# Kernel tuning notes

Hardware: AMD Instinct MI355X
Metric: run time of the kernel (lower is better)

## Reference

```python
import jax, jax.numpy as jnp
import numpy as np


def setup_inputs() -> dict:
    key = jax.random.key(0)
    kx, ky = jax.random.split(key)
    N, M, D = 16384, 16384, 512
    x = jax.random.normal(kx, (N, D), dtype=jnp.float32)
    y = jax.random.normal(ky, (M, D), dtype=jnp.float32)
    return {"x": x, "y": y, "device": 0}


def reference(x, y, device):
    # torch.cdist(x, y, p=2): pairwise Euclidean distances [N, M]
    # matching torch's large-matrix cdist path), clamped for numerical safety.
    x_sq = jnp.sum(x * x, axis=1, keepdims=True)          # [N, 1]
    y_sq = jnp.sum(y * y, axis=1)                          # [M]
    sq_dists = x_sq + y_sq[None, :] - 2.0 * (x @ y.T)      # [N, M]
    dists = jnp.sqrt(jnp.maximum(sq_dists, 0.0))
    # min over centers (dim=1), then argmax over candidates (dim=0)
    min_dists = jnp.min(dists, axis=1)                     # [N]
    max_id = jnp.argmax(min_dists)
    max_val = min_dists[max_id]
    return max_val, max_id
```

## Files before the change

### kernel.cpp

```cpp
#include <hip/hip_runtime.h>
#include <hip/hip_fp8.h>
#include <math.h>

#define N_ROWS 16384
#define M_ROWS 16384
#define DIM    512
#define JS     8
#define KCAND  256
#define DELTA  0.40f

typedef __attribute__((ext_vector_type(8))) int   int8v;
typedef __attribute__((ext_vector_type(4))) int   int4v;
typedef __attribute__((ext_vector_type(4))) float floatx4;

__global__ __launch_bounds__(256) void convert_kernel(const float* __restrict__ x, const float* __restrict__ y,
                                                      unsigned char* __restrict__ xh8, unsigned char* __restrict__ yh8,
                                                      float* __restrict__ x_sq, float* __restrict__ y_sq,
                                                      unsigned int* __restrict__ gmax_bits,
                                                      unsigned int* __restrict__ cnt, int* __restrict__ cand) {
    if (blockIdx.x == 0) {
        if (threadIdx.x < KCAND) cand[threadIdx.x] = 0;
        if (threadIdx.x == 0) { *gmax_bits = 0u; *cnt = 0u; }
    }
    int wave = threadIdx.x >> 6, lane = threadIdx.x & 63;
    int row = blockIdx.x * 4 + wave;
    const float* src; unsigned char* dst8; float* dsq; int r;
    if (row < N_ROWS) { r = row;          src = x; dst8 = xh8; dsq = x_sq; }
    else              { r = row - N_ROWS; src = y; dst8 = yh8; dsq = y_sq; }
    const float4* s4 = (const float4*)(src + (size_t)r * DIM);
    float4 a = s4[lane * 2];
    float4 b = s4[lane * 2 + 1];
    float v[8] = {a.x, a.y, a.z, a.w, b.x, b.y, b.z, b.w};
    union { unsigned char b[8]; uint2 u2; } pk;
    float s = 0.f;
    #pragma unroll
    for (int i = 0; i < 8; ++i) {
        s += v[i] * v[i];
        __hip_fp8_e4m3 q(v[i]);
        pk.b[i] = (unsigned char)q.__x;
    }
    *(uint2*)(dst8 + (size_t)r * DIM + lane * 8) = pk.u2;
    #pragma unroll
    for (int off = 32; off > 0; off >>= 1) s += __shfl_down(s, off, 64);
    if (lane == 0) dsq[r] = s;
}

__device__ __forceinline__ int8v read_frag(const unsigned char* base, int row, int quad) {
    int s = row & 7;
    int c0 = ((quad << 1) | 0) ^ s;
    int c1 = ((quad << 1) | 1) ^ s;
    int4v lo = *(const int4v*)(base + row * 128 + c0 * 16);
    int4v hi = *(const int4v*)(base + row * 128 + c1 * 16);
    int8v r;
    r[0] = lo[0]; r[1] = lo[1]; r[2] = lo[2]; r[3] = lo[3];
    r[4] = hi[0]; r[5] = hi[1]; r[6] = hi[2]; r[7] = hi[3];
    return r;
}

__global__ __launch_bounds__(256) void pass1_kernel(const unsigned char* __restrict__ xh8,
                                                    const unsigned char* __restrict__ yh8,
                                                    const float* __restrict__ y_sq,
                                                    float* __restrict__ part) {
    __shared__ __align__(16) unsigned char As[128 * 128];
    __shared__ __align__(16) unsigned char Bs[128 * 128];
    __shared__ float red[2][128];

    const int t = threadIdx.x;
    const int wid = t >> 6, lane = t & 63;
    const int wm = wid >> 1, wn = wid & 1;
    const int col = lane & 15, quad = lane >> 4;
    const int i0 = blockIdx.x * 128;
    const int jsplit = blockIdx.y;

    const unsigned char* sSrc = (wid < 2) ? xh8 : yh8;
    unsigned char* sDst = (wid < 2) ? As : Bs;
    const int sBase = (wid & 1) * 64;
    const int rr = lane >> 3;
    const int p  = lane & 7;
    const int srcChunkOff = ((p ^ rr) << 4);

    float minv[16];
    #pragma unroll
    for (int i = 0; i < 16; ++i) minv[i] = __builtin_inff();

    for (int jt = 0; jt < (M_ROWS / JS) / 128; ++jt) {
        const int j0 = jsplit * (M_ROWS / JS) + jt * 128;
        const int gBase = (wid < 2) ? i0 : j0;
        floatx4 acc[4][4];
        #pragma unroll
        for (int mt = 0; mt < 4; ++mt)
            #pragma unroll
            for (int nt = 0; nt < 4; ++nt) acc[mt][nt] = (floatx4){0.f, 0.f, 0.f, 0.f};

        for (int kc = 0; kc < DIM; kc += 128) {
            #pragma unroll
            for (int r = 0; r < 8; ++r) {
                const unsigned char* gp = sSrc + (size_t)(gBase + sBase + r * 8 + rr) * DIM + kc + srcChunkOff;
                unsigned char* lp = sDst + (sBase + r * 8) * 128;
                __builtin_amdgcn_global_load_lds((const __attribute__((address_space(1))) void*)gp,
                                                 (__attribute__((address_space(3))) void*)lp, 16, 0, 0);
            }
            __syncthreads();
            int8v afr[4], bfr[4];
            #pragma unroll
            for (int mt = 0; mt < 4; ++mt) afr[mt] = read_frag(As, wm * 64 + mt * 16 + col, quad);
            #pragma unroll
            for (int nt = 0; nt < 4; ++nt) bfr[nt] = read_frag(Bs, wn * 64 + nt * 16 + col, quad);
            #pragma unroll
            for (int mt = 0; mt < 4; ++mt)
                #pragma unroll
                for (int nt = 0; nt < 4; ++nt)
                    acc[mt][nt] = __builtin_amdgcn_mfma_scale_f32_16x16x128_f8f6f4(
                        afr[mt], bfr[nt], acc[mt][nt],
                        0, 0,
                        0, 127,
                        0, 127);
            __syncthreads();
        }
        #pragma unroll
        for (int nt = 0; nt < 4; ++nt) {
            float q = y_sq[j0 + wn * 64 + nt * 16 + col];
            #pragma unroll
            for (int mt = 0; mt < 4; ++mt)
                #pragma unroll
                for (int r = 0; r < 4; ++r)
                    minv[mt * 4 + r] = fminf(minv[mt * 4 + r], q - 2.f * acc[mt][nt][r]);
        }
    }

    #pragma unroll
    for (int i = 0; i < 16; ++i) {
        float v = minv[i];
        v = fminf(v, __shfl_xor(v, 1, 64));
        v = fminf(v, __shfl_xor(v, 2, 64));
        v = fminf(v, __shfl_xor(v, 4, 64));
        v = fminf(v, __shfl_xor(v, 8, 64));
        minv[i] = v;
    }
    if (col == 0) {
        #pragma unroll
        for (int mt = 0; mt < 4; ++mt)
            #pragma unroll
            for (int r = 0; r < 4; ++r)
                red[wn][wm * 64 + mt * 16 + quad * 4 + r] = minv[mt * 4 + r];
    }
    __syncthreads();
    if (t < 128)
        part[(size_t)(i0 + t) * JS + jsplit] = fminf(red[0][t], red[1][t]);
}

__global__ __launch_bounds__(1024) void maxred_kernel(const float* __restrict__ part,
                                                      const float* __restrict__ x_sq,
                                                      float* __restrict__ aval,
                                                      unsigned int* __restrict__ gmax_bits) {
    __shared__ float sm[1024];
    int t = threadIdx.x;
    int row = blockIdx.x * 1024 + t;
    float m = part[(size_t)row * JS];
    #pragma unroll
    for (int c = 1; c < JS; ++c) m = fminf(m, part[(size_t)row * JS + c]);
    float v = sqrtf(fmaxf(x_sq[row] + m, 0.f));
    aval[row] = v;
    sm[t] = v;
    __syncthreads();
    for (int s = 512; s > 0; s >>= 1) {
        if (t < s) sm[t] = fmaxf(sm[t], sm[t + s]);
        __syncthreads();
    }
    if (t == 0) atomicMax(gmax_bits, __float_as_uint(sm[0]));
}

__global__ __launch_bounds__(1024) void select_kernel(const float* __restrict__ aval,
                                                      const unsigned int* __restrict__ gmax_bits,
                                                      unsigned int* __restrict__ cnt,
                                                      int* __restrict__ cand) {
    int row = blockIdx.x * 1024 + threadIdx.x;
    float gmax = __uint_as_float(*gmax_bits);
    if (aval[row] >= gmax - DELTA) {
        unsigned s = atomicAdd(cnt, 1u);
        if (s < KCAND) cand[s] = row;
    }
}

#define TIr 64
#define LDA 68
#define LDB 132
__global__ __launch_bounds__(256) void rescore_kernel(const float* __restrict__ x, const float* __restrict__ y,
                                                      const float* __restrict__ y_sq,
                                                      const int* __restrict__ cand,
                                                      const unsigned int* __restrict__ cnt,
                                                      float* __restrict__ part2) {
    __shared__ __align__(16) float As[32 * LDA];
    __shared__ __align__(16) float Bs[32 * LDB];
    __shared__ float red[TIr][17];

    int t = threadIdx.x;
    int tx = t & 15, ty = t >> 4;
    int i0 = blockIdx.x * TIr;
    int j0 = blockIdx.y * 128;

    if ((unsigned)i0 >= *cnt) return;

    float acc[4][8];
    #pragma unroll
    for (int c = 0; c < 4; ++c)
        #pragma unroll
        for (int d = 0; d < 8; ++d) acc[c][d] = 0.f;

    int srow = t >> 3;
    int skq = (t & 7) * 4;
    int grow0 = cand[i0 + srow];
    int grow1 = cand[i0 + 32 + srow];

    for (int kc = 0; kc < DIM; kc += 32) {
        {
            float4 v = *(const float4*)(x + (size_t)grow0 * DIM + kc + skq);
            As[(skq + 0) * LDA + srow] = v.x;
            As[(skq + 1) * LDA + srow] = v.y;
            As[(skq + 2) * LDA + srow] = v.z;
            As[(skq + 3) * LDA + srow] = v.w;
            v = *(const float4*)(x + (size_t)grow1 * DIM + kc + skq);
            As[(skq + 0) * LDA + 32 + srow] = v.x;
            As[(skq + 1) * LDA + 32 + srow] = v.y;
            As[(skq + 2) * LDA + 32 + srow] = v.z;
            As[(skq + 3) * LDA + 32 + srow] = v.w;
        }
        #pragma unroll
        for (int it = 0; it < 4; ++it) {
            int row = it * 32 + srow;
            float4 v = *(const float4*)(y + (size_t)(j0 + row) * DIM + kc + skq);
            Bs[(skq + 0) * LDB + row] = v.x;
            Bs[(skq + 1) * LDB + row] = v.y;
            Bs[(skq + 2) * LDB + row] = v.z;
            Bs[(skq + 3) * LDB + row] = v.w;
        }
        __syncthreads();
        #pragma unroll 8
        for (int k = 0; k < 32; ++k) {
            float4 a  = *(const float4*)&As[k * LDA + ty * 4];
            float4 b0 = *(const float4*)&Bs[k * LDB + tx * 8];
            float4 b1 = *(const float4*)&Bs[k * LDB + tx * 8 + 4];
            float av[4] = {a.x, a.y, a.z, a.w};
            float bv[8] = {b0.x, b0.y, b0.z, b0.w, b1.x, b1.y, b1.z, b1.w};
            #pragma unroll
            for (int c = 0; c < 4; ++c)
                #pragma unroll
                for (int d = 0; d < 8; ++d)
                    acc[c][d] = fmaf(av[c], bv[d], acc[c][d]);
        }
        __syncthreads();
    }

    float4 q0 = *(const float4*)(y_sq + j0 + tx * 8);
    float4 q1 = *(const float4*)(y_sq + j0 + tx * 8 + 4);
    float qv[8] = {q0.x, q0.y, q0.z, q0.w, q1.x, q1.y, q1.z, q1.w};
    float mv[4] = {__builtin_inff(), __builtin_inff(), __builtin_inff(), __builtin_inff()};
    #pragma unroll
    for (int c = 0; c < 4; ++c)
        #pragma unroll
        for (int d = 0; d < 8; ++d)
            mv[c] = fminf(mv[c], qv[d] - 2.f * acc[c][d]);
    #pragma unroll
    for (int c = 0; c < 4; ++c) red[ty * 4 + c][tx] = mv[c];
    __syncthreads();
    if (t < TIr) {
        float m = red[t][0];
        #pragma unroll
        for (int xx = 1; xx < 16; ++xx) m = fminf(m, red[t][xx]);
        part2[(size_t)(i0 + t) * 128 + blockIdx.y] = m;
    }
}

__global__ __launch_bounds__(256) void final2_kernel(const float* __restrict__ part2,
                                                     const float* __restrict__ x_sq,
                                                     const int* __restrict__ cand,
                                                     const unsigned int* __restrict__ cnt,
                                                     float* __restrict__ out) {
    __shared__ float sv[256];
    __shared__ int si[256];
    int t = threadIdx.x;
    const float4* p4 = (const float4*)(part2 + (size_t)t * 128);
    float m = __builtin_inff();
    for (int c = 0; c < 32; ++c) {
        float4 v = p4[c];
        m = fminf(m, fminf(fminf(v.x, v.y), fminf(v.z, v.w)));
    }
    unsigned n = *cnt;
    if (n > KCAND) n = KCAND;
    int row = cand[t];
    float v = (t < (int)n) ? sqrtf(fmaxf(x_sq[row] + m, 0.f)) : -__builtin_inff();
    sv[t] = v; si[t] = row;
    __syncthreads();
    for (int s = 128; s > 0; s >>= 1) {
        if (t < s) {
            float v2 = sv[t + s]; int i2 = si[t + s];
            if (v2 > sv[t] || (v2 == sv[t] && i2 < si[t])) { sv[t] = v2; si[t] = i2; }
        }
        __syncthreads();
    }
    if (t == 0) { out[0] = sv[0]; out[1] = (float)si[0]; }
}

extern "C" void kernel_launch(void* const* d_in, const int* in_sizes, int n_in,
                              void* d_out, int out_size, void* d_ws, size_t ws_size,
                              hipStream_t stream) {
    const float* x = (const float*)d_in[0];
    const float* y = (const float*)d_in[1];
    float* out = (float*)d_out;

    char* w = (char*)d_ws;
    unsigned char* xh8 = (unsigned char*)w;
    unsigned char* yh8 = (unsigned char*)(w + (size_t)8388608);
    float* x_sq = (float*)(w + (size_t)16777216);
    float* y_sq = x_sq + N_ROWS;
    float* part = y_sq + M_ROWS;
    float* aval = part + (size_t)N_ROWS * JS;
    float* part2 = aval + N_ROWS;
    int* cand = (int*)(part2 + KCAND * 128);
    unsigned int* gmax_bits = (unsigned int*)(cand + KCAND);
    unsigned int* cnt = gmax_bits + 1;

    convert_kernel<<<(N_ROWS + M_ROWS) / 4, 256, 0, stream>>>(x, y, xh8, yh8, x_sq, y_sq, gmax_bits, cnt, cand);
    dim3 g1(N_ROWS / 128, JS);
    pass1_kernel<<<g1, 256, 0, stream>>>(xh8, yh8, y_sq, part);
    maxred_kernel<<<N_ROWS / 1024, 1024, 0, stream>>>(part, x_sq, aval, gmax_bits);
    select_kernel<<<N_ROWS / 1024, 1024, 0, stream>>>(aval, gmax_bits, cnt, cand);
    dim3 g2(KCAND / TIr, M_ROWS / 128);
    rescore_kernel<<<g2, 256, 0, stream>>>(x, y, y_sq, cand, cnt, part2);
    final2_kernel<<<1, 256, 0, stream>>>(part2, x_sq, cand, cnt, out);
}
```

Before: 323.5 us.

## Keep A fragments in registers and pipeline B tiles through 4-stage LDS ring

```diff
diff --git a/kernel.cpp b/kernel.cpp
--- a/kernel.cpp
+++ b/kernel.cpp
@@ -45,88 +45,124 @@
     if (lane == 0) dsq[r] = s;
 }
 
-__device__ __forceinline__ int8v read_frag(const unsigned char* base, int row, int quad) {
-    int s = row & 7;
-    int c0 = ((quad << 1) | 0) ^ s;
-    int c1 = ((quad << 1) | 1) ^ s;
-    int4v lo = *(const int4v*)(base + row * 128 + c0 * 16);
-    int4v hi = *(const int4v*)(base + row * 128 + c1 * 16);
-    int8v r;
-    r[0] = lo[0]; r[1] = lo[1]; r[2] = lo[2]; r[3] = lo[3];
-    r[4] = hi[0]; r[5] = hi[1]; r[6] = hi[2]; r[7] = hi[3];
-    return r;
-}
-
-__global__ __launch_bounds__(256) void pass1_kernel(const unsigned char* __restrict__ xh8,
-                                                    const unsigned char* __restrict__ yh8,
-                                                    const float* __restrict__ y_sq,
-                                                    float* __restrict__ part) {
-    __shared__ __align__(16) unsigned char As[128 * 128];
-    __shared__ __align__(16) unsigned char Bs[128 * 128];
-    __shared__ float red[2][128];
+__global__ __launch_bounds__(256, 2) void pass1_kernel(const unsigned char* __restrict__ xh8,
+                                                       const unsigned char* __restrict__ yh8,
+                                                       const float* __restrict__ y_sq,
+                                                       float* __restrict__ part) {
+    __shared__ __align__(16) unsigned char Bs[4][16384];
+    __shared__ __align__(16) float ysq_s[M_ROWS / JS];
+    __shared__ float red[4][64];
 
     const int t = threadIdx.x;
-    const int wid = t >> 6, lane = t & 63;
-    const int wm = wid >> 1, wn = wid & 1;
-    const int col = lane & 15, quad = lane >> 4;
-    const int i0 = blockIdx.x * 128;
-    const int jsplit = blockIdx.y;
-
-    const unsigned char* sSrc = (wid < 2) ? xh8 : yh8;
-    unsigned char* sDst = (wid < 2) ? As : Bs;
-    const int sBase = (wid & 1) * 64;
-    const int rr = lane >> 3;
-    const int p  = lane & 7;
-    const int srcChunkOff = ((p ^ rr) << 4);
+    const int w = t >> 6, lane = t & 63;
+    const int col = lane & 15, q = lane >> 4;
+
+    const int bid = blockIdx.x;
+    const int wg = (bid & 7) * 256 + (bid >> 3);
+    const int js = wg >> 8;
+    const int i0 = (wg & 255) * 64;
+    const int jbase = js * (M_ROWS / JS);
+
+    {
+        const float4* ys4 = (const float4*)(y_sq + jbase);
+        float4 v0 = ys4[t * 2];
+        float4 v1 = ys4[t * 2 + 1];
+        *(float4*)&ysq_s[t * 8]     = v0;
+        *(float4*)&ysq_s[t * 8 + 4] = v1;
+    }
+
+    int8v afr[4][4];
+    {
+        const unsigned char* ab = xh8 + (size_t)(i0 + col) * DIM + q * 32;
+        #pragma unroll
+        for (int mt = 0; mt < 4; ++mt)
+            #pragma unroll
+            for (int kc = 0; kc < 4; ++kc) {
+                const int4v* p = (const int4v*)(ab + mt * 16 * DIM + kc * 128);
+                int4v a0 = p[0], a1 = p[1];
+                int8v f;
+                f[0] = a0[0]; f[1] = a0[1]; f[2] = a0[2]; f[3] = a0[3];
+                f[4] = a1[0]; f[5] = a1[1]; f[6] = a1[2]; f[7] = a1[3];
+                afr[mt][kc] = f;
+            }
+    }
+
+    const unsigned char* sp[4];
+    {
+        const unsigned char* tb = yh8 + (size_t)jbase * DIM;
+        #pragma unroll
+        for (int i = 0; i < 4; ++i) {
+            int s  = w * 256 + i * 64 + lane;
+            int g  = s >> 7, u = s & 127;
+            int jl = (g << 4) + (u & 15);
+            int c  = (u >> 4) ^ (u & 7);
+            sp[i] = tb + jl * DIM + c * 16;
+        }
+    }
+    const int Klane = col * 16 + (((q << 1) ^ (col & 7)) << 8);
 
     float minv[16];
     #pragma unroll
     for (int i = 0; i < 16; ++i) minv[i] = __builtin_inff();
 
-    for (int jt = 0; jt < (M_ROWS / JS) / 128; ++jt) {
-        const int j0 = jsplit * (M_ROWS / JS) + jt * 128;
-        const int gBase = (wid < 2) ? i0 : j0;
-        floatx4 acc[4][4];
-        #pragma unroll
-        for (int mt = 0; mt < 4; ++mt)
-            #pragma unroll
-            for (int nt = 0; nt < 4; ++nt) acc[mt][nt] = (floatx4){0.f, 0.f, 0.f, 0.f};
-
-        for (int kc = 0; kc < DIM; kc += 128) {
-            #pragma unroll
-            for (int r = 0; r < 8; ++r) {
-                const unsigned char* gp = sSrc + (size_t)(gBase + sBase + r * 8 + rr) * DIM + kc + srcChunkOff;
-                unsigned char* lp = sDst + (sBase + r * 8) * 128;
-                __builtin_amdgcn_global_load_lds((const __attribute__((address_space(1))) void*)gp,
-                                                 (__attribute__((address_space(3))) void*)lp, 16, 0, 0);
-            }
-            __syncthreads();
-            int8v afr[4], bfr[4];
-            #pragma unroll
-            for (int mt = 0; mt < 4; ++mt) afr[mt] = read_frag(As, wm * 64 + mt * 16 + col, quad);
-            #pragma unroll
-            for (int nt = 0; nt < 4; ++nt) bfr[nt] = read_frag(Bs, wn * 64 + nt * 16 + col, quad);
-            #pragma unroll
-            for (int mt = 0; mt < 4; ++mt)
+    __syncthreads();
+
+#define STAGE(BUF, TOFF)                                                                     \
+    { _Pragma("unroll")                                                                      \
+      for (int i_ = 0; i_ < 4; ++i_) {                                                       \
+          __builtin_amdgcn_global_load_lds(                                                  \
+              (const __attribute__((address_space(1))) void*)(sp[i_] + (TOFF)),              \
+              (__attribute__((address_space(3))) void*)(&Bs[BUF][w * 4096 + i_ * 1024]),     \
+              16, 0, 0);                                                                     \
+      } }
+
+    STAGE(0, 0)
+    STAGE(1, 128)
+
+    for (int jt = 0; jt < 16; ++jt) {
+        floatx4 acc[4][2];
+        #pragma unroll
+        for (int mt = 0; mt < 4; ++mt) {
+            acc[mt][0] = (floatx4){0.f, 0.f, 0.f, 0.f};
+            acc[mt][1] = (floatx4){0.f, 0.f, 0.f, 0.f};
+        }
+        #pragma unroll
+        for (int kc = 0; kc < 4; ++kc) {
+            const int toff = (jt + (kc >> 1)) * (128 * DIM) + (((kc + 2) & 3) << 7);
+            STAGE((kc + 2) & 3, toff)
+            asm volatile("s_waitcnt vmcnt(8)" ::: "memory");
+            __builtin_amdgcn_s_barrier();
+            asm volatile("" ::: "memory");
+            #pragma unroll
+            for (int nt = 0; nt < 2; ++nt) {
+                const unsigned char* gb = &Bs[kc][(w * 2 + nt) * 2048];
+                int4v lo = *(const int4v*)(gb + Klane);
+                int4v hi = *(const int4v*)(gb + (Klane ^ 256));
+                int8v b;
+                b[0] = lo[0]; b[1] = lo[1]; b[2] = lo[2]; b[3] = lo[3];
+                b[4] = hi[0]; b[5] = hi[1]; b[6] = hi[2]; b[7] = hi[3];
+                __builtin_amdgcn_s_setprio(1);
                 #pragma unroll
-                for (int nt = 0; nt < 4; ++nt)
+                for (int mt = 0; mt < 4; ++mt)
                     acc[mt][nt] = __builtin_amdgcn_mfma_scale_f32_16x16x128_f8f6f4(
-                        afr[mt], bfr[nt], acc[mt][nt],
+                        afr[mt][kc], b, acc[mt][nt],
                         0, 0,
                         0, 127,
                         0, 127);
-            __syncthreads();
-        }
-        #pragma unroll
-        for (int nt = 0; nt < 4; ++nt) {
-            float q = y_sq[j0 + wn * 64 + nt * 16 + col];
+                __builtin_amdgcn_s_setprio(0);
+            }
+        }
+        #pragma unroll
+        for (int nt = 0; nt < 2; ++nt) {
+            float qv = ysq_s[jt * 128 + w * 32 + nt * 16 + col];
             #pragma unroll
             for (int mt = 0; mt < 4; ++mt)
                 #pragma unroll
                 for (int r = 0; r < 4; ++r)
-                    minv[mt * 4 + r] = fminf(minv[mt * 4 + r], q - 2.f * acc[mt][nt][r]);
-        }
-    }
+                    minv[mt * 4 + r] = fminf(minv[mt * 4 + r], qv - 2.f * acc[mt][nt][r]);
+        }
+    }
+#undef STAGE
 
     #pragma unroll
     for (int i = 0; i < 16; ++i) {
@@ -142,11 +178,12 @@
         for (int mt = 0; mt < 4; ++mt)
             #pragma unroll
             for (int r = 0; r < 4; ++r)
-                red[wn][wm * 64 + mt * 16 + quad * 4 + r] = minv[mt * 4 + r];
-    }
-    __syncthreads();
-    if (t < 128)
-        part[(size_t)(i0 + t) * JS + jsplit] = fminf(red[0][t], red[1][t]);
+                red[w][mt * 16 + q * 4 + r] = minv[mt * 4 + r];
+    }
+    __syncthreads();
+    if (t < 64)
+        part[(size_t)(i0 + t) * JS + js] =
+            fminf(fminf(red[0][t], red[1][t]), fminf(red[2][t], red[3][t]));
 }
 
 __global__ __launch_bounds__(1024) void maxred_kernel(const float* __restrict__ part,
@@ -321,8 +358,7 @@
     unsigned int* cnt = gmax_bits + 1;
 
     convert_kernel<<<(N_ROWS + M_ROWS) / 4, 256, 0, stream>>>(x, y, xh8, yh8, x_sq, y_sq, gmax_bits, cnt, cand);
-    dim3 g1(N_ROWS / 128, JS);
-    pass1_kernel<<<g1, 256, 0, stream>>>(xh8, yh8, y_sq, part);
+    pass1_kernel<<<2048, 256, 0, stream>>>(xh8, yh8, y_sq, part);
     maxred_kernel<<<N_ROWS / 1024, 1024, 0, stream>>>(part, x_sq, aval, gmax_bits);
     select_kernel<<<N_ROWS / 1024, 1024, 0, stream>>>(aval, gmax_bits, cnt, cand);
     dim3 g2(KCAND / TIr, M_ROWS / 128);
```

Result: no change. 321.4 us (-0.7%).
